# Optimization experiments

Hardware: AMD Instinct MI355X
Metric: run time of the kernel (lower is better)

## Reference

```python
import jax, jax.numpy as jnp
import numpy as np

B, S, H, D = 4, 2048, 12, 64
HID = H * D  # 768
EPS = 1e-5


def _layer_norm(h, w, b):
    mu = jnp.mean(h, axis=-1, keepdims=True)
    var = jnp.mean((h - mu) ** 2, axis=-1, keepdims=True)
    return w * (h - mu) / jnp.sqrt(var + EPS) + b


def setup_inputs() -> dict:
    key = jax.random.key(0)
    ks = jax.random.split(key, 12)
    sc = 1.0 / np.sqrt(HID)
    inp = {
        "x": jax.random.normal(ks[0], (B, S, HID), jnp.float32),
        "ln1_w": jnp.ones((HID,), jnp.float32),
        "ln1_b": jnp.zeros((HID,), jnp.float32),
        "Wq": jax.random.normal(ks[1], (HID, HID), jnp.float32) * sc,
        "bq": jnp.zeros((HID,), jnp.float32),
        "Wk": jax.random.normal(ks[2], (HID, HID), jnp.float32) * sc,
        "bk": jnp.zeros((HID,), jnp.float32),
        "Wv": jax.random.normal(ks[3], (HID, HID), jnp.float32) * sc,
        "bv": jnp.zeros((HID,), jnp.float32),
        "Wo": jax.random.normal(ks[4], (HID, HID), jnp.float32) * sc,
        "bo": jnp.zeros((HID,), jnp.float32),
        "ln2_w": jnp.ones((HID,), jnp.float32),
        "ln2_b": jnp.zeros((HID,), jnp.float32),
        "W1": jax.random.normal(ks[5], (HID, 4 * HID), jnp.float32) * sc,
        "b1": jnp.zeros((4 * HID,), jnp.float32),
        "W2": jax.random.normal(ks[6], (4 * HID, HID), jnp.float32) * (1.0 / np.sqrt(4 * HID)),
        "b2": jnp.zeros((HID,), jnp.float32),
    }
    return inp


def _split_heads(t):
    # (B, S, H*D) -> (B, H, S, D)
    b, s, _ = t.shape
    return t.reshape(b, s, H, -1).transpose(0, 2, 1, 3)


def _merge_heads(t):
    # (B, H, S, D) -> (B, S, H*D)
    b, h, s, d = t.shape
    return t.transpose(0, 2, 1, 3).reshape(b, s, h * d)


def _attention(h, Wq, bq, Wk, bk, Wv, bv, Wo, bo):
    q = _split_heads(h @ Wq + bq)  # (B,H,S,D)
    k = _split_heads(h @ Wk + bk)
    v = _split_heads(h @ Wv + bv)
    scores = jnp.einsum("bhqd,bhkd->bhqk", q, k) / jnp.sqrt(jnp.asarray(D, h.dtype))
    causal = jnp.tril(jnp.ones((q.shape[2], q.shape[2]), bool))  # (S,S)
    scores = jnp.where(causal, scores, jnp.finfo(scores.dtype).min)
    w = jax.nn.softmax(scores, axis=-1)
    out = jnp.einsum("bhqk,bhkd->bhqd", w, v)
    return _merge_heads(out) @ Wo + bo


def reference(x, ln1_w, ln1_b, Wq, bq, Wk, bk, Wv, bv, Wo, bo, ln2_w, ln2_b, W1, b1, W2, b2):
    # Pre-LN transformer block: x + attn(LN(x)); then x + MLP(LN(x))
    a = _attention(_layer_norm(x, ln1_w, ln1_b), Wq, bq, Wk, bk, Wv, bv, Wo, bo)
    x = x + a
    h = _layer_norm(x, ln2_w, ln2_b)
    m = jax.nn.gelu(h @ W1 + b1, approximate=False) @ W2 + b2
    return x + m
```

## Files before the change

### kernel.cpp

```cpp
#include <hip/hip_runtime.h>
#include <cmath>
#include <stdint.h>

typedef unsigned short u16;
typedef __attribute__((ext_vector_type(8))) short short8;
typedef __attribute__((ext_vector_type(4))) float f32x4;
typedef __attribute__((ext_vector_type(4))) unsigned int u32x4;

#define HID 768
#define FF  3072
#define SEQ 2048
#define NHEAD 12
#define NROWS 8192

__device__ __forceinline__ float bf2f(u16 u){ return __uint_as_float(((unsigned)u)<<16); }
__device__ __forceinline__ u16 f2bf(float f){
  unsigned x = __float_as_uint(f);
  x += 0x7fffu + ((x>>16)&1u);
  return (u16)(x>>16);
}
__device__ __forceinline__ unsigned cvtpk(float a, float b){
  unsigned r;
  asm("v_cvt_pk_bf16_f32 %0, %1, %2" : "=v"(r) : "v"(a), "v"(b));
  return r;
}
__device__ __forceinline__ void gload16(const void* g, void* l){
  __builtin_amdgcn_global_load_lds((const __attribute__((address_space(1))) unsigned*)g,
                                   (__attribute__((address_space(3))) unsigned*)l, 16, 0, 0);
}

__global__ __launch_bounds__(256) void wconv(const float* __restrict__ in,
                                             u16* __restrict__ out, int K, int N)
{
  __shared__ float t[32][33];
  const int bk = blockIdx.x*32, bn = blockIdx.y*32;
  const int tn = threadIdx.x & 31, tk = threadIdx.x >> 5;
  #pragma unroll
  for (int j=0;j<4;++j)
    t[tk+8*j][tn] = in[(size_t)(bk+tk+8*j)*N + bn + tn];
  __syncthreads();
  #pragma unroll
  for (int j=0;j<4;++j)
    out[(size_t)(bn+tk+8*j)*K + bk + tn] = f2bf(t[tn][tk+8*j]);
}

__global__ __launch_bounds__(256) void tconv(const u16* __restrict__ in,
                                             u16* __restrict__ out, int K, int N)
{
  __shared__ u16 t[32][34];
  const int bk = blockIdx.x*32, bn = blockIdx.y*32;
  const int tn = threadIdx.x & 31, tk = threadIdx.x >> 5;
  #pragma unroll
  for (int j=0;j<4;++j)
    t[tk+8*j][tn] = in[(size_t)(bk+tk+8*j)*N + bn + tn];
  __syncthreads();
  #pragma unroll
  for (int j=0;j<4;++j)
    out[(size_t)(bn+tk+8*j)*K + bk + tn] = t[tn][tk+8*j];
}

__global__ __launch_bounds__(256) void ln_k(const float* __restrict__ in,
    const float* __restrict__ gw, const float* __restrict__ gb,
    u16* __restrict__ out)
{
  const int row = blockIdx.x*4 + (threadIdx.x>>6);
  const int l = threadIdx.x & 63;
  const float* p = in + (size_t)row*HID;
  float4 v[3];
  float s=0.f, ss=0.f;
  #pragma unroll
  for (int j=0;j<3;++j){
    v[j] = *(const float4*)(p + j*256 + l*4);
    s  += v[j].x + v[j].y + v[j].z + v[j].w;
    ss += v[j].x*v[j].x + v[j].y*v[j].y + v[j].z*v[j].z + v[j].w*v[j].w;
  }
  #pragma unroll
  for (int m=1;m<64;m<<=1){
    s  += __shfl_xor(s,  m, 64);
    ss += __shfl_xor(ss, m, 64);
  }
  const float mu = s * (1.f/768.f);
  const float rstd = rsqrtf(ss*(1.f/768.f) - mu*mu + 1e-5f);
  #pragma unroll
  for (int j=0;j<3;++j){
    const float4 wv = *(const float4*)(gw + j*256 + l*4);
    const float4 bv = *(const float4*)(gb + j*256 + l*4);
    ushort4 o;
    o.x = f2bf((v[j].x-mu)*rstd*wv.x + bv.x);
    o.y = f2bf((v[j].y-mu)*rstd*wv.y + bv.y);
    o.z = f2bf((v[j].z-mu)*rstd*wv.z + bv.z);
    o.w = f2bf((v[j].w-mu)*rstd*wv.w + bv.w);
    *(ushort4*)(out + (size_t)row*HID + j*256 + l*4) = o;
  }
}

template<int MODE, int BN>
__global__ __launch_bounds__(256) void gemm_bt(const u16* __restrict__ A,
    const u16* __restrict__ Bt, const float* __restrict__ bias0,
    const float* __restrict__ bias1, const float* __restrict__ bias2,
    const float* __restrict__ res, void* __restrict__ outp,
    int N, int K, long wstride, long ostride)
{
  constexpr int NI = BN/32;
  __shared__ __align__(16) u16 sA[2][128*32];
  __shared__ __align__(16) u16 sB[2][BN*32];
  const int tid = threadIdx.x, l = tid&63, w = tid>>6;
  const int wr = w>>1, wc = w&1, hi = l>>4, lo = l&15;
  const int bm = blockIdx.x*128, bn = blockIdx.y*BN;
  const int z = blockIdx.z;
  const u16* Bz = Bt + (size_t)z * (size_t)wstride;
  const float* bias = (z==0) ? bias0 : ((z==1)? bias1 : bias2);

  const u16* Arow = A  + (size_t)bm*K;
  const u16* Brow = Bz + (size_t)bn*K;

  const f32x4 zv = {0.f,0.f,0.f,0.f};
  f32x4 acc[4][NI];
  #pragma unroll
  for (int i=0;i<4;++i)
    #pragma unroll
    for (int j=0;j<NI;++j) acc[i][j] = zv;

  const int r0_ = tid>>2, off_ = (tid&3)*8;
  const int r1_ = r0_ + 64;

  gload16(Arow + (size_t)r0_*K + off_, (char*)sA[0] + tid*16);
  gload16(Arow + (size_t)r1_*K + off_, (char*)sA[0] + (tid+256)*16);
  gload16(Brow + (size_t)r0_*K + off_, (char*)sB[0] + tid*16);
  if constexpr (BN==128)
    gload16(Brow + (size_t)r1_*K + off_, (char*)sB[0] + (tid+256)*16);
  __syncthreads();

  const int NT = K >> 5;
  int cur = 0;
  for (int t=0; t<NT; ++t){
    if (t+1 < NT){
      const int kt = (t+1) << 5;
      gload16(Arow + (size_t)r0_*K + kt + off_, (char*)sA[cur^1] + tid*16);
      gload16(Arow + (size_t)r1_*K + kt + off_, (char*)sA[cur^1] + (tid+256)*16);
      gload16(Brow + (size_t)r0_*K + kt + off_, (char*)sB[cur^1] + tid*16);
      if constexpr (BN==128)
        gload16(Brow + (size_t)r1_*K + kt + off_, (char*)sB[cur^1] + (tid+256)*16);
    }
    short8 af[4], bfv[NI];
    #pragma unroll
    for (int i=0;i<4;++i)
      af[i]  = *(const short8*)(sA[cur] + (wr*64 + i*16 + lo)*32 + hi*8);
    #pragma unroll
    for (int i=0;i<NI;++i)
      bfv[i] = *(const short8*)(sB[cur] + (wc*(BN/2) + i*16 + lo)*32 + hi*8);
    #pragma unroll
    for (int mi=0;mi<4;++mi)
      #pragma unroll
      for (int ni=0;ni<NI;++ni)
        acc[mi][ni] = __builtin_amdgcn_mfma_f32_16x16x32_bf16(af[mi], bfv[ni], acc[mi][ni], 0,0,0);
    __syncthreads();
    cur ^= 1;
  }

  #pragma unroll
  for (int mi=0;mi<4;++mi)
    #pragma unroll
    for (int ni=0;ni<NI;++ni){
      const int r0 = bm + wr*64 + mi*16 + 4*hi;
      const int cc = bn + wc*(BN/2) + ni*16 + lo;
      const float bv = bias[cc];
      #pragma unroll
      for (int g=0; g<4; ++g){
        const size_t idx = (size_t)(r0+g)*N + cc;
        float v = acc[mi][ni][g] + bv;
        if (MODE == 0){
          ((u16*)outp + (size_t)z*(size_t)ostride)[idx] = f2bf(v);
        } else if (MODE == 1){
          ((float*)outp)[idx] = res[idx] + v;
        } else {
          float u = v*(0.7978845608f + 0.0356774081f*v*v);
          float e = __expf(2.f*u);
          float th = 1.f - 2.f/(1.f + e);
          ((u16*)outp)[idx] = f2bf(0.5f*v*(1.f + th));
        }
      }
    }
}

__global__ __launch_bounds__(256, 4) void attn_k(const u16* __restrict__ Qm,
                                                 const u16* __restrict__ Km,
                                                 const u16* __restrict__ Vt,
                                                 u16* __restrict__ Om)
{
  __shared__ __align__(16) u16 sK [64*64];
  __shared__ __align__(16) u16 sVT[64*64];
  const int tid = threadIdx.x, l = tid & 63, w = tid >> 6;
  const int hi = l >> 4, lo = l & 15;
  const int idx = blockIdx.x;
  const int qb = 31 - (idx / 48);
  const int bh = idx % 48;
  const int b = bh / NHEAD, h = bh - (bh / NHEAD) * NHEAD;
  const size_t rb = (size_t)b * SEQ;
  const int qw = qb*64 + w*16;

  short8 qf[2];
  #pragma unroll
  for (int ks=0; ks<2; ++ks){
    short8 t = *(const short8*)(Qm + (rb + qw + lo)*HID + h*64 + ks*32 + hi*8);
    #pragma unroll
    for (int i=0;i<8;++i) t[i] = (short)f2bf(bf2f((u16)t[i]) * 0.1803368801f);
    qf[ks] = t;
  }

  const f32x4 zv = {0.f,0.f,0.f,0.f};
  f32x4 oa[4] = {zv, zv, zv, zv};
  float m = -INFINITY, lsum = 0.f;
  const int srcA = (((2*hi)  & 3) << 4) | lo;
  const int srcB = (((2*hi+1)& 3) << 4) | lo;

  for (int t=0; t<=qb; ++t){
    const int kv0 = t*64;
    __syncthreads();
    #pragma unroll
    for (int j=0;j<2;++j){
      int c = tid + 256*j;
      int row = c >> 3;
      int d0 = ((c&7) ^ (row&7))*8;
      gload16(Km + (rb + kv0 + row)*HID + h*64 + d0, (char*)sK + c*16);
    }
    #pragma unroll
    for (int j=0;j<2;++j){
      int c = tid + 256*j;
      int row = c >> 3;
      int k0 = ((c&7) ^ (row&7))*8;
      gload16(Vt + (size_t)(h*64 + row)*NROWS + rb + kv0 + k0, (char*)sVT + c*16);
    }
    __syncthreads();

    f32x4 sc[4] = {zv, zv, zv, zv};
    #pragma unroll
    for (int ks=0;ks<2;++ks){
      #pragma unroll
      for (int ni=0;ni<4;++ni){
        short8 kf = *(const short8*)(sK + (ni*16 + lo)*64 + ((ks*32 + hi*8) ^ ((lo&7)*8)));
        sc[ni] = __builtin_amdgcn_mfma_f32_16x16x32_bf16(kf, qf[ks], sc[ni], 0,0,0);
      }
    }

    if (t == qb){
      #pragma unroll
      for (int ni=0;ni<4;++ni)
        #pragma unroll
        for (int g=0; g<4; ++g){
          int kg = kv0 + ni*16 + 4*hi + g;
          if (kg > qw + lo) sc[ni][g] = -INFINITY;
        }
    }

    float a0 = fmaxf(fmaxf(sc[0][0], sc[0][1]), fmaxf(sc[0][2], sc[0][3]));
    float a1 = fmaxf(fmaxf(sc[1][0], sc[1][1]), fmaxf(sc[1][2], sc[1][3]));
    float a2 = fmaxf(fmaxf(sc[2][0], sc[2][1]), fmaxf(sc[2][2], sc[2][3]));
    float a3 = fmaxf(fmaxf(sc[3][0], sc[3][1]), fmaxf(sc[3][2], sc[3][3]));
    float pm = fmaxf(fmaxf(a0, a1), fmaxf(a2, a3));
    pm = fmaxf(pm, __shfl_xor(pm, 16, 64));
    pm = fmaxf(pm, __shfl_xor(pm, 32, 64));

    if (!__all(pm - m <= 10.f)){
      const float mnew = fmaxf(m, pm);
      const float alpha = __builtin_amdgcn_exp2f(m - mnew);
      lsum *= alpha;
      #pragma unroll
      for (int nd=0;nd<4;++nd){
        oa[nd][0]*=alpha; oa[nd][1]*=alpha; oa[nd][2]*=alpha; oa[nd][3]*=alpha;
      }
      m = mnew;
    }

    float ps = 0.f;
    #pragma unroll
    for (int ni=0;ni<4;++ni)
      #pragma unroll
      for (int g=0; g<4; ++g){
        float e = __builtin_amdgcn_exp2f(sc[ni][g] - m);
        sc[ni][g] = e;
        ps += e;
      }
    ps += __shfl_xor(ps, 16, 64);
    ps += __shfl_xor(ps, 32, 64);
    lsum += ps;

    #pragma unroll
    for (int ks=0;ks<2;++ks){
      unsigned pkA0 = cvtpk(sc[2*ks  ][0], sc[2*ks  ][1]);
      unsigned pkA1 = cvtpk(sc[2*ks  ][2], sc[2*ks  ][3]);
      unsigned pkB0 = cvtpk(sc[2*ks+1][0], sc[2*ks+1][1]);
      unsigned pkB1 = cvtpk(sc[2*ks+1][2], sc[2*ks+1][3]);
      unsigned a0u = (unsigned)__shfl((int)pkA0, srcA, 64);
      unsigned b0u = (unsigned)__shfl((int)pkB0, srcA, 64);
      unsigned a1u = (unsigned)__shfl((int)pkA1, srcA, 64);
      unsigned b1u = (unsigned)__shfl((int)pkB1, srcA, 64);
      unsigned a2u = (unsigned)__shfl((int)pkA0, srcB, 64);
      unsigned b2u = (unsigned)__shfl((int)pkB0, srcB, 64);
      unsigned a3u = (unsigned)__shfl((int)pkA1, srcB, 64);
      unsigned b3u = (unsigned)__shfl((int)pkB1, srcB, 64);
      union { u32x4 u; short8 s; } pf;
      pf.u = (u32x4){ (hi<2)?a0u:b0u, (hi<2)?a1u:b1u, (hi<2)?a2u:b2u, (hi<2)?a3u:b3u };

      #pragma unroll
      for (int nd=0;nd<4;++nd){
        short8 vf = *(const short8*)(sVT + (nd*16 + lo)*64 + ((ks*32 + hi*8) ^ ((lo&7)*8)));
        oa[nd] = __builtin_amdgcn_mfma_f32_16x16x32_bf16(vf, pf.s, oa[nd], 0,0,0);
      }
    }
  }

  const float inv = 1.f / lsum;
  #pragma unroll
  for (int nd=0;nd<4;++nd){
    ushort4 o;
    o.x = f2bf(oa[nd][0]*inv);
    o.y = f2bf(oa[nd][1]*inv);
    o.z = f2bf(oa[nd][2]*inv);
    o.w = f2bf(oa[nd][3]*inv);
    *(ushort4*)(Om + (rb + qw + lo)*HID + h*64 + nd*16 + 4*hi) = o;
  }
}

extern "C" void kernel_launch(void* const* d_in, const int* in_sizes, int n_in,
                              void* d_out, int out_size, void* d_ws, size_t ws_size,
                              hipStream_t stream)
{
  const float* x    = (const float*)d_in[0];
  const float* ln1w = (const float*)d_in[1];
  const float* ln1b = (const float*)d_in[2];
  const float* Wq   = (const float*)d_in[3];
  const float* bq   = (const float*)d_in[4];
  const float* Wk   = (const float*)d_in[5];
  const float* bk   = (const float*)d_in[6];
  const float* Wv   = (const float*)d_in[7];
  const float* bv   = (const float*)d_in[8];
  const float* Wo   = (const float*)d_in[9];
  const float* bo   = (const float*)d_in[10];
  const float* ln2w = (const float*)d_in[11];
  const float* ln2b = (const float*)d_in[12];
  const float* W1   = (const float*)d_in[13];
  const float* b1   = (const float*)d_in[14];
  const float* W2   = (const float*)d_in[15];
  const float* b2   = (const float*)d_in[16];

  u16* wq_t = (u16*)d_ws;
  u16* wk_t = wq_t + 589824;
  u16* wv_t = wk_t + 589824;
  u16* wo_t = wv_t + 589824;
  u16* w1_t = wo_t + 589824;
  u16* w2_t = w1_t + 2359296;
  u16* hbf  = w2_t + 2359296;
  u16* qb_  = hbf + 6291456;
  u16* kb_  = qb_ + 6291456;
  u16* vb_  = kb_ + 6291456;
  u16* atb  = vb_ + 6291456;
  u16* ub   = qb_;
  float* x2 = (float*)(atb + 6291456);

  const size_t need = 102236160ull;
  if (ws_size < need) return;

  dim3 blk(256);
  wconv<<<dim3(24,24), blk, 0, stream>>>(Wq, wq_t, 768, 768);
  wconv<<<dim3(24,24), blk, 0, stream>>>(Wk, wk_t, 768, 768);
  wconv<<<dim3(24,24), blk, 0, stream>>>(Wv, wv_t, 768, 768);
  wconv<<<dim3(24,24), blk, 0, stream>>>(Wo, wo_t, 768, 768);
  wconv<<<dim3(24,96), blk, 0, stream>>>(W1, w1_t, 768, 3072);
  wconv<<<dim3(96,24), blk, 0, stream>>>(W2, w2_t, 3072, 768);

  ln_k<<<2048, blk, 0, stream>>>(x, ln1w, ln1b, hbf);

  gemm_bt<0,64><<<dim3(64,12,3), blk, 0, stream>>>(hbf, wq_t, bq, bk, bv,
      nullptr, (void*)qb_, 768, 768, 589824L, 6291456L);
  tconv<<<dim3(256,24), blk, 0, stream>>>(vb_, hbf, 8192, 768);

  attn_k<<<dim3(1536), blk, 0, stream>>>(qb_, kb_, hbf, atb);

  gemm_bt<1,64><<<dim3(64,12,1), blk, 0, stream>>>(atb, wo_t, bo, bo, bo,
      x, (void*)x2, 768, 768, 0L, 0L);

  ln_k<<<2048, blk, 0, stream>>>(x2, ln2w, ln2b, hbf);

  gemm_bt<2,128><<<dim3(64,24,1), blk, 0, stream>>>(hbf, w1_t, b1, b1, b1,
      nullptr, (void*)ub, 3072, 768, 0L, 0L);

  gemm_bt<1,64><<<dim3(64,12,1), blk, 0, stream>>>(ub, w2_t, b2, b2, b2,
      x2, d_out, 768, 3072, 0L, 0L);
}
```

Baseline: 397.4 us.

## Triple-buffer GEMM shared-memory pipeline and use 128x128 tiles for all GEMMs

```diff
diff --git a/kernel.cpp b/kernel.cpp
--- a/kernel.cpp
+++ b/kernel.cpp
@@ -94,19 +94,18 @@
   }
 }
 
-template<int MODE, int BN>
+template<int MODE>
 __global__ __launch_bounds__(256) void gemm_bt(const u16* __restrict__ A,
     const u16* __restrict__ Bt, const float* __restrict__ bias0,
     const float* __restrict__ bias1, const float* __restrict__ bias2,
     const float* __restrict__ res, void* __restrict__ outp,
     int N, int K, long wstride, long ostride)
 {
-  constexpr int NI = BN/32;
-  __shared__ __align__(16) u16 sA[2][128*32];
-  __shared__ __align__(16) u16 sB[2][BN*32];
+  __shared__ __align__(16) u16 sA[3][128*32];
+  __shared__ __align__(16) u16 sB[3][128*32];
   const int tid = threadIdx.x, l = tid&63, w = tid>>6;
   const int wr = w>>1, wc = w&1, hi = l>>4, lo = l&15;
-  const int bm = blockIdx.x*128, bn = blockIdx.y*BN;
+  const int bm = blockIdx.x*128, bn = blockIdx.y*128;
   const int z = blockIdx.z;
   const u16* Bz = Bt + (size_t)z * (size_t)wstride;
   const float* bias = (z==0) ? bias0 : ((z==1)? bias1 : bias2);
@@ -115,55 +114,61 @@
   const u16* Brow = Bz + (size_t)bn*K;
 
   const f32x4 zv = {0.f,0.f,0.f,0.f};
-  f32x4 acc[4][NI];
+  f32x4 acc[4][4];
   #pragma unroll
   for (int i=0;i<4;++i)
     #pragma unroll
-    for (int j=0;j<NI;++j) acc[i][j] = zv;
+    for (int j=0;j<4;++j) acc[i][j] = zv;
 
   const int r0_ = tid>>2, off_ = (tid&3)*8;
   const int r1_ = r0_ + 64;
 
-  gload16(Arow + (size_t)r0_*K + off_, (char*)sA[0] + tid*16);
-  gload16(Arow + (size_t)r1_*K + off_, (char*)sA[0] + (tid+256)*16);
-  gload16(Brow + (size_t)r0_*K + off_, (char*)sB[0] + tid*16);
-  if constexpr (BN==128)
-    gload16(Brow + (size_t)r1_*K + off_, (char*)sB[0] + (tid+256)*16);
-  __syncthreads();
+  #define STAGE(T, BUF) do { \
+    const int kt_ = (T) << 5; \
+    gload16(Arow + (size_t)r0_*K + kt_ + off_, (char*)sA[BUF] + tid*16); \
+    gload16(Arow + (size_t)r1_*K + kt_ + off_, (char*)sA[BUF] + (tid+256)*16); \
+    gload16(Brow + (size_t)r0_*K + kt_ + off_, (char*)sB[BUF] + tid*16); \
+    gload16(Brow + (size_t)r1_*K + kt_ + off_, (char*)sB[BUF] + (tid+256)*16); \
+  } while(0)
 
   const int NT = K >> 5;
+  STAGE(0, 0);
+  STAGE(1, 1);
+  asm volatile("s_waitcnt vmcnt(4)" ::: "memory");
+  __builtin_amdgcn_s_barrier();
+  __builtin_amdgcn_sched_barrier(0);
+
   int cur = 0;
   for (int t=0; t<NT; ++t){
+    int nb = cur+2; if (nb>=3) nb-=3;
+    if (t+2 < NT) STAGE(t+2, nb);
+    short8 af[4], bfv[4];
+    #pragma unroll
+    for (int i=0;i<4;++i){
+      af[i]  = *(const short8*)(sA[cur] + (wr*64 + i*16 + lo)*32 + hi*8);
+      bfv[i] = *(const short8*)(sB[cur] + (wc*64 + i*16 + lo)*32 + hi*8);
+    }
+    #pragma unroll
+    for (int mi=0;mi<4;++mi)
+      #pragma unroll
+      for (int ni=0;ni<4;++ni)
+        acc[mi][ni] = __builtin_amdgcn_mfma_f32_16x16x32_bf16(af[mi], bfv[ni], acc[mi][ni], 0,0,0);
     if (t+1 < NT){
-      const int kt = (t+1) << 5;
-      gload16(Arow + (size_t)r0_*K + kt + off_, (char*)sA[cur^1] + tid*16);
-      gload16(Arow + (size_t)r1_*K + kt + off_, (char*)sA[cur^1] + (tid+256)*16);
-      gload16(Brow + (size_t)r0_*K + kt + off_, (char*)sB[cur^1] + tid*16);
-      if constexpr (BN==128)
-        gload16(Brow + (size_t)r1_*K + kt + off_, (char*)sB[cur^1] + (tid+256)*16);
-    }
-    short8 af[4], bfv[NI];
-    #pragma unroll
-    for (int i=0;i<4;++i)
-      af[i]  = *(const short8*)(sA[cur] + (wr*64 + i*16 + lo)*32 + hi*8);
-    #pragma unroll
-    for (int i=0;i<NI;++i)
-      bfv[i] = *(const short8*)(sB[cur] + (wc*(BN/2) + i*16 + lo)*32 + hi*8);
-    #pragma unroll
-    for (int mi=0;mi<4;++mi)
-      #pragma unroll
-      for (int ni=0;ni<NI;++ni)
-        acc[mi][ni] = __builtin_amdgcn_mfma_f32_16x16x32_bf16(af[mi], bfv[ni], acc[mi][ni], 0,0,0);
-    __syncthreads();
-    cur ^= 1;
-  }
+      if (t+2 < NT) asm volatile("s_waitcnt vmcnt(4)" ::: "memory");
+      else          asm volatile("s_waitcnt vmcnt(0)" ::: "memory");
+      __builtin_amdgcn_s_barrier();
+      __builtin_amdgcn_sched_barrier(0);
+    }
+    cur = (cur+1==3) ? 0 : cur+1;
+  }
+  #undef STAGE
 
   #pragma unroll
   for (int mi=0;mi<4;++mi)
     #pragma unroll
-    for (int ni=0;ni<NI;++ni){
+    for (int ni=0;ni<4;++ni){
       const int r0 = bm + wr*64 + mi*16 + 4*hi;
-      const int cc = bn + wc*(BN/2) + ni*16 + lo;
+      const int cc = bn + wc*64 + ni*16 + lo;
       const float bv = bias[cc];
       #pragma unroll
       for (int g=0; g<4; ++g){
@@ -371,20 +376,20 @@
 
   ln_k<<<2048, blk, 0, stream>>>(x, ln1w, ln1b, hbf);
 
-  gemm_bt<0,64><<<dim3(64,12,3), blk, 0, stream>>>(hbf, wq_t, bq, bk, bv,
+  gemm_bt<0><<<dim3(64,6,3), blk, 0, stream>>>(hbf, wq_t, bq, bk, bv,
       nullptr, (void*)qb_, 768, 768, 589824L, 6291456L);
   tconv<<<dim3(256,24), blk, 0, stream>>>(vb_, hbf, 8192, 768);
 
   attn_k<<<dim3(1536), blk, 0, stream>>>(qb_, kb_, hbf, atb);
 
-  gemm_bt<1,64><<<dim3(64,12,1), blk, 0, stream>>>(atb, wo_t, bo, bo, bo,
+  gemm_bt<1><<<dim3(64,6,1), blk, 0, stream>>>(atb, wo_t, bo, bo, bo,
       x, (void*)x2, 768, 768, 0L, 0L);
 
   ln_k<<<2048, blk, 0, stream>>>(x2, ln2w, ln2b, hbf);
 
-  gemm_bt<2,128><<<dim3(64,24,1), blk, 0, stream>>>(hbf, w1_t, b1, b1, b1,
+  gemm_bt<2><<<dim3(64,24,1), blk, 0, stream>>>(hbf, w1_t, b1, b1, b1,
       nullptr, (void*)ub, 3072, 768, 0L, 0L);
 
-  gemm_bt<1,64><<<dim3(64,12,1), blk, 0, stream>>>(ub, w2_t, b2, b2, b2,
+  gemm_bt<1><<<dim3(64,6,1), blk, 0, stream>>>(ub, w2_t, b2, b2, b2,
       x2, d_out, 768, 3072, 0L, 0L);
 }
```

Measured after the change: 404.7 us. Within noise of the previous version (+1.8%).
